# Optimization experiments

Hardware: AMD Instinct MI355X
Metric: run time of the kernel (lower is better)

Reference implementation:

```python
import jax, jax.numpy as jnp
import numpy as np

N_NODES = 50000
N_EDGES = 800000
IN_DIM = 128
HID = 256
OUT_DIM = 256
N_HEADS = 8
E_DIM = 64
KV_IN = 2 * IN_DIM + E_DIM  # 320


def _mlp_params(key, din, dhid, dout):
    k1, k2 = jax.random.split(key)
    s1 = 1.0 / np.sqrt(din)
    s2 = 1.0 / np.sqrt(dhid)
    return (jax.random.uniform(k1, (din, dhid), jnp.float32, -s1, s1),
            jnp.zeros((dhid,), jnp.float32),
            jax.random.uniform(k2, (dhid, dout), jnp.float32, -s2, s2),
            jnp.zeros((dout,), jnp.float32))


def setup_inputs() -> dict:
    key = jax.random.key(0)
    kh, ke, kidx, kk, kv, kq = jax.random.split(key, 6)
    h = jax.random.normal(kh, (N_NODES, IN_DIM), jnp.float32)
    e = jax.random.normal(ke, (N_EDGES, E_DIM), jnp.float32)
    edge_index = jax.random.randint(kidx, (2, N_EDGES), 0, N_NODES, jnp.int64)
    Wk1, bk1, Wk2, bk2 = _mlp_params(kk, KV_IN, HID, OUT_DIM)
    Wv1, bv1, Wv2, bv2 = _mlp_params(kv, KV_IN, HID, OUT_DIM)
    Wq1, bq1, Wq2, bq2 = _mlp_params(kq, IN_DIM, HID, OUT_DIM)
    return {"h": h, "e": e, "edge_index": edge_index,
            "Wk1": Wk1, "bk1": bk1, "Wk2": Wk2, "bk2": bk2,
            "Wv1": Wv1, "bv1": bv1, "Wv2": Wv2, "bv2": bv2,
            "Wq1": Wq1, "bq1": bq1, "Wq2": Wq2, "bq2": bq2}


def _mlp(x, W1, b1, W2, b2):
    # MLP(in, out, hidden, norm=False): Linear -> ReLU -> Linear
    return jax.nn.relu(x @ W1 + b1) @ W2 + b2


def reference(h, e, edge_index,
              Wk1, bk1, Wk2, bk2,
              Wv1, bv1, Wv2, bv2,
              Wq1, bq1, Wq2, bq2):
    N = h.shape[0]
    d_head = OUT_DIM // N_HEADS
    src, dst = edge_index[0], edge_index[1]
    # gather endpoints: hi = h[dst], hj = h[src]
    kv_input = jnp.concatenate([e, h[dst], h[src]], axis=-1)  # [E, KV_IN]
    k = _mlp(kv_input, Wk1, bk1, Wk2, bk2).reshape(-1, N_HEADS, d_head)
    v = _mlp(kv_input, Wv1, bv1, Wv2, bv2).reshape(-1, N_HEADS, d_head)
    q = _mlp(h, Wq1, bq1, Wq2, bq2).reshape(-1, N_HEADS, d_head)
    # per-edge logits, scaled dot product [E, H]
    logits = jnp.sum(q[dst] * k, axis=-1) * (1.0 / np.sqrt(d_head))
    # scatter softmax over destination groups
    mx = jax.ops.segment_max(logits, dst, num_segments=N)  # [N, H]
    ex = jnp.exp(logits - mx[dst])
    den = jax.ops.segment_sum(ex, dst, num_segments=N)  # [N, H]
    alpha = ex / den[dst]  # [E, H]
    # weighted scatter-sum aggregate
    m = alpha[..., None] * v  # [E, H, d_head]
    out = jax.ops.segment_sum(m, dst, num_segments=N)  # [N, H, d_head]
    return out.reshape(N, OUT_DIM)
```

## Files before the change

### kernel.cpp

```cpp
#include <hip/hip_runtime.h>

#define NND 50000
#define NE  800000
#define IND 128
#define HD  256
#define OD  256
#define NH  8
#define ED  64

typedef __attribute__((ext_vector_type(8))) short bf16x8;
typedef __attribute__((ext_vector_type(4))) float f32x4;

__device__ __forceinline__ float bf2f(unsigned short u) {
    union { unsigned int i; float f; } x; x.i = ((unsigned int)u) << 16; return x.f;
}
__device__ __forceinline__ unsigned short f2bf(float f) {
    union { float f; unsigned int i; } x; x.f = f;
    unsigned int u = x.i;
    u += 0x7FFFu + ((u >> 16) & 1u);
    return (unsigned short)(u >> 16);
}
__device__ __forceinline__ unsigned int pk2(float a, float b) {
    unsigned int r;
    asm("v_cvt_pk_bf16_f32 %0, %1, %2" : "=v"(r) : "v"(a), "v"(b));
    return r;
}

__global__ void k_hist(const int* __restrict__ eidx, int* __restrict__ cnt) {
    int e = blockIdx.x * 256 + threadIdx.x;
    if (e < NE) atomicAdd(&cnt[eidx[NE + e]], 1);
}

__global__ __launch_bounds__(1024) void k_scan(const int* __restrict__ cnt,
                                               int* __restrict__ head) {
    __shared__ int part[1024];
    const int t = threadIdx.x;
    const int CH = (NND + 1023) / 1024;
    int base = t * CH;
    int s = 0;
    for (int i = 0; i < CH; ++i) { int idx = base + i; if (idx < NND) s += cnt[idx]; }
    part[t] = s;
    __syncthreads();
    for (int off = 1; off < 1024; off <<= 1) {
        int v = (t >= off) ? part[t - off] : 0;
        __syncthreads();
        part[t] += v;
        __syncthreads();
    }
    int excl = (t == 0) ? 0 : part[t - 1];
    for (int i = 0; i < CH; ++i) {
        int idx = base + i; if (idx >= NND) break;
        head[idx] = excl;
        excl += cnt[idx];
    }
}

__global__ void k_scatter(const int* __restrict__ eidx, int* __restrict__ head,
                          int* __restrict__ perm, int* __restrict__ srcS,
                          int* __restrict__ dstS) {
    int e = blockIdx.x * 256 + threadIdx.x;
    if (e < NE) {
        int s = eidx[e];
        int d = eidx[NE + e];
        int pos = atomicAdd(&head[d], 1);
        perm[pos] = e;
        srcS[pos] = s;
        dstS[pos] = d;
    }
}

__device__ __forceinline__ void pack1(const float* __restrict__ W,
                                      unsigned short* __restrict__ P,
                                      int K, int N, int rowoff, int tid) {
    int j = tid & 7;
    int l = (tid >> 3) & 63;
    int rest = tid >> 9;
    int KS = K >> 5;
    int ks = rest % KS;
    int ct = rest / KS;
    int n = ct * 16 + (l & 15);
    int k = ks * 32 + (l >> 4) * 8 + j;
    P[tid] = f2bf(W[(size_t)(rowoff + k) * N + n]);
}

__global__ void k_packall(const float* __restrict__ Wq1, const float* __restrict__ Wq2,
                          const float* __restrict__ Wk1, const float* __restrict__ Wk2,
                          const float* __restrict__ Wv1, const float* __restrict__ Wv2,
                          unsigned short* __restrict__ Wq1p, unsigned short* __restrict__ Wq2p,
                          unsigned short* __restrict__ WeK,  unsigned short* __restrict__ W2K,
                          unsigned short* __restrict__ WdK,  unsigned short* __restrict__ WsK,
                          unsigned short* __restrict__ WeV,  unsigned short* __restrict__ W2V,
                          unsigned short* __restrict__ WdV,  unsigned short* __restrict__ WsV)
{
    int tid = blockIdx.x * 256 + threadIdx.x;
    int chunk = tid >> 14;
    if      (chunk < 2)   pack1(Wq1, Wq1p, 128, 256, 0,   tid);
    else if (chunk < 6)   pack1(Wq2, Wq2p, 256, 256, 0,   tid - (2 << 14));
    else if (chunk < 7)   pack1(Wk1, WeK,   64, 256, 0,   tid - (6 << 14));
    else if (chunk < 11)  pack1(Wk2, W2K,  256, 256, 0,   tid - (7 << 14));
    else if (chunk < 13)  pack1(Wk1, WdK,  128, 256, 64,  tid - (11 << 14));
    else if (chunk < 15)  pack1(Wk1, WsK,  128, 256, 192, tid - (13 << 14));
    else if (chunk < 16)  pack1(Wv1, WeV,   64, 256, 0,   tid - (15 << 14));
    else if (chunk < 20)  pack1(Wv2, W2V,  256, 256, 0,   tid - (16 << 14));
    else if (chunk < 22)  pack1(Wv1, WdV,  128, 256, 64,  tid - (20 << 14));
    else                  pack1(Wv1, WsV,  128, 256, 192, tid - (22 << 14));
}

__device__ __forceinline__ void zero_acc(f32x4 (&acc)[4][4]) {
    #pragma unroll
    for (int c = 0; c < 4; ++c)
        #pragma unroll
        for (int i = 0; i < 4; ++i)
            #pragma unroll
            for (int r = 0; r < 4; ++r) acc[c][i][r] = 0.f;
}

template<int KS, int STRIDE>
__device__ __forceinline__ void gemmT(const unsigned short* X,
                                      const unsigned short* __restrict__ Wp,
                                      int w, int l, f32x4 (&acc)[4][4]) {
    for (int ks = 0; ks < KS; ++ks) {
        bf16x8 wf[4], xf[4];
        #pragma unroll
        for (int c = 0; c < 4; ++c)
            wf[c] = *(const bf16x8*)(Wp + (((4 * w + c) * KS + ks) * 64 + l) * 8);
        #pragma unroll
        for (int i = 0; i < 4; ++i)
            xf[i] = *(const bf16x8*)(X + (i * 16 + (l & 15)) * STRIDE + ks * 32 + (l >> 4) * 8);
        #pragma unroll
        for (int c = 0; c < 4; ++c)
            #pragma unroll
            for (int i = 0; i < 4; ++i)
                acc[c][i] = __builtin_amdgcn_mfma_f32_16x16x32_bf16(wf[c], xf[i], acc[c][i], 0, 0, 0);
    }
}

__device__ __forceinline__ void lin_epi(const unsigned short* __restrict__ Wp,
                                        unsigned short* __restrict__ outp,
                                        const unsigned short* sXp,
                                        int w, int l, int g, int el, int m0) {
    f32x4 acc[4][4];
    zero_acc(acc);
    gemmT<4, 136>(sXp, Wp, w, l, acc);
    #pragma unroll
    for (int c = 0; c < 4; ++c) {
        int hid0 = 64 * w + 16 * c + 4 * g;
        #pragma unroll
        for (int i = 0; i < 4; ++i) {
            int node = m0 + 16 * i + el;
            if (node < NND) {
                uint2 pk;
                pk.x = pk2(acc[c][i][0], acc[c][i][1]);
                pk.y = pk2(acc[c][i][2], acc[c][i][3]);
                *(uint2*)(outp + (size_t)node * HD + hid0) = pk;
            }
        }
    }
}

__global__ __launch_bounds__(256) void k_node(
    const float* __restrict__ h,
    const unsigned short* __restrict__ Wq1p, const float* __restrict__ bq1,
    const unsigned short* __restrict__ Wq2p, const float* __restrict__ bq2,
    unsigned short* __restrict__ qb,
    const unsigned short* __restrict__ WdK, const unsigned short* __restrict__ WsK,
    const unsigned short* __restrict__ WdV, const unsigned short* __restrict__ WsV,
    unsigned short* __restrict__ udK, unsigned short* __restrict__ usK,
    unsigned short* __restrict__ udV, unsigned short* __restrict__ usV)
{
    __shared__ unsigned short sX[64][136];
    __shared__ unsigned short sH[64][264];
    const int t = threadIdx.x, w = t >> 6, l = t & 63;
    const int g = l >> 4, el = l & 15;
    const int m0 = blockIdx.x * 64;

    for (int c = t; c < 2048; c += 256) {
        int row = c >> 5, j = c & 31;
        int node = m0 + row; if (node >= NND) node = NND - 1;
        float4 v = *(const float4*)(h + (size_t)node * IND + j * 4);
        uint2 pk; pk.x = pk2(v.x, v.y); pk.y = pk2(v.z, v.w);
        *(uint2*)(&sX[row][j * 4]) = pk;
    }
    __syncthreads();

    f32x4 acc[4][4];
    zero_acc(acc);
    gemmT<4, 136>(&sX[0][0], Wq1p, w, l, acc);
    #pragma unroll
    for (int c = 0; c < 4; ++c) {
        int hid0 = 64 * w + 16 * c + 4 * g;
        float4 bv = *(const float4*)(bq1 + hid0);
        #pragma unroll
        for (int i = 0; i < 4; ++i) {
            uint2 pk;
            pk.x = pk2(fmaxf(acc[c][i][0] + bv.x, 0.f), fmaxf(acc[c][i][1] + bv.y, 0.f));
            pk.y = pk2(fmaxf(acc[c][i][2] + bv.z, 0.f), fmaxf(acc[c][i][3] + bv.w, 0.f));
            *(uint2*)(&sH[16 * i + el][hid0]) = pk;
        }
    }
    __syncthreads();

    zero_acc(acc);
    gemmT<8, 264>(&sH[0][0], Wq2p, w, l, acc);
    #pragma unroll
    for (int c = 0; c < 4; ++c) {
        int out0 = 64 * w + 16 * c + 4 * g;
        float4 bv = *(const float4*)(bq2 + out0);
        #pragma unroll
        for (int i = 0; i < 4; ++i) {
            int node = m0 + 16 * i + el;
            if (node < NND) {
                uint2 pk;
                pk.x = pk2(acc[c][i][0] + bv.x, acc[c][i][1] + bv.y);
                pk.y = pk2(acc[c][i][2] + bv.z, acc[c][i][3] + bv.w);
                *(uint2*)(qb + (size_t)node * OD + out0) = pk;
            }
        }
    }

    lin_epi(WdK, udK, &sX[0][0], w, l, g, el, m0);
    lin_epi(WsK, usK, &sX[0][0], w, l, g, el, m0);
    lin_epi(WdV, udV, &sX[0][0], w, l, g, el, m0);
    lin_epi(WsV, usV, &sX[0][0], w, l, g, el, m0);
}

struct SmF {
    unsigned short E[64][72];
    unsigned short H[64][264];
    int   Eid[64];
    int   Src[64];
    int   Dst[64];
    float Ex[64][9];
};

__device__ __forceinline__ void epi_pre(SmF& sm, f32x4 (&acc)[4][4],
                                        const float* __restrict__ b1,
                                        int w, int g, int el) {
    #pragma unroll
    for (int c = 0; c < 4; ++c) {
        int hid0 = 64 * w + 16 * c + 4 * g;
        float4 bv = *(const float4*)(b1 + hid0);
        #pragma unroll
        for (int i = 0; i < 4; ++i) {
            uint2 pk;
            pk.x = pk2(acc[c][i][0] + bv.x, acc[c][i][1] + bv.y);
            pk.y = pk2(acc[c][i][2] + bv.z, acc[c][i][3] + bv.w);
            *(uint2*)(&sm.H[16 * i + el][hid0]) = pk;
        }
    }
}

__device__ __forceinline__ void elemwise(SmF& sm,
                                         const unsigned short* __restrict__ ud,
                                         const unsigned short* __restrict__ us,
                                         int t) {
    int er = t >> 2;
    const unsigned short* udr = ud + (size_t)sm.Dst[er] * HD;
    const unsigned short* usr = us + (size_t)sm.Src[er] * HD;
    bf16x8 vd[8], vs[8];
    #pragma unroll
    for (int j = 0; j < 8; ++j) {
        int col = (j * 4 + (t & 3)) * 8;
        vd[j] = *(const bf16x8*)(udr + col);
        vs[j] = *(const bf16x8*)(usr + col);
    }
    #pragma unroll
    for (int j = 0; j < 8; ++j) {
        int col = (j * 4 + (t & 3)) * 8;
        bf16x8 hv = *(const bf16x8*)(&sm.H[er][col]);
        float x[8];
        #pragma unroll
        for (int u = 0; u < 8; ++u) {
            x[u] = bf2f((unsigned short)hv[u]) + bf2f((unsigned short)vd[j][u])
                 + bf2f((unsigned short)vs[j][u]);
            x[u] = fmaxf(x[u], 0.f);
        }
        uint4 o;
        o.x = pk2(x[0], x[1]); o.y = pk2(x[2], x[3]);
        o.z = pk2(x[4], x[5]); o.w = pk2(x[6], x[7]);
        *(uint4*)(&sm.H[er][col]) = o;
    }
}

__global__ __launch_bounds__(256, 3) void k_edgeF(
    const float* __restrict__ eattr,
    const int* __restrict__ perm,
    const int* __restrict__ srcS, const int* __restrict__ dstS,
    const unsigned short* __restrict__ WeK, const float* __restrict__ b1K,
    const unsigned short* __restrict__ W2K, const float* __restrict__ b2K,
    const unsigned short* __restrict__ WeV, const float* __restrict__ b1V,
    const unsigned short* __restrict__ W2V, const float* __restrict__ b2V,
    const unsigned short* __restrict__ udK, const unsigned short* __restrict__ usK,
    const unsigned short* __restrict__ udV, const unsigned short* __restrict__ usV,
    const unsigned short* __restrict__ qb,
    float* __restrict__ den, float* __restrict__ outp)
{
    __shared__ SmF sm;
    const int t = threadIdx.x, w = t >> 6, l = t & 63;
    const int g = l >> 4, el = l & 15;
    const int e0 = blockIdx.x * 64;

    if (t < 64) {
        sm.Eid[t] = perm[e0 + t];
        sm.Src[t] = srcS[e0 + t];
        sm.Dst[t] = dstS[e0 + t];
    }
    __syncthreads();
    for (int c = t; c < 1024; c += 256) {
        int row = c >> 4, j = c & 15;
        float4 v = *(const float4*)(eattr + (size_t)sm.Eid[row] * ED + j * 4);
        uint2 pk; pk.x = pk2(v.x, v.y); pk.y = pk2(v.z, v.w);
        *(uint2*)(&sm.E[row][j * 4]) = pk;
    }
    __syncthreads();

    f32x4 acc[4][4];

    zero_acc(acc);
    gemmT<2, 72>(&sm.E[0][0], WeK, w, l, acc);
    epi_pre(sm, acc, b1K, w, g, el);
    __syncthreads();
    elemwise(sm, udK, usK, t);
    __syncthreads();

    zero_acc(acc);
    gemmT<8, 264>(&sm.H[0][0], W2K, w, l, acc);
    __syncthreads();
    epi_pre(sm, acc, b2K, w, g, el);
    __syncthreads();

    {
        const float scale = 0.17677669529663687f;
        for (int p = t; p < 512; p += 256) {
            int er = p >> 3, hh = p & 7;
            int dn = sm.Dst[er];
            const unsigned short* qrow = qb + (size_t)dn * OD + hh * 32;
            float s = 0.f;
            #pragma unroll
            for (int jj = 0; jj < 32; jj += 8) {
                bf16x8 qv = *(const bf16x8*)(qrow + jj);
                bf16x8 kv = *(const bf16x8*)(&sm.H[er][hh * 32 + jj]);
                #pragma unroll
                for (int u = 0; u < 8; ++u)
                    s += bf2f((unsigned short)qv[u]) * bf2f((unsigned short)kv[u]);
            }
            float ex = __expf(s * scale);
            sm.Ex[er][hh] = ex;
            atomicAdd(&den[dn * NH + hh], ex);
        }
    }

    zero_acc(acc);
    gemmT<2, 72>(&sm.E[0][0], WeV, w, l, acc);
    __syncthreads();
    epi_pre(sm, acc, b1V, w, g, el);
    __syncthreads();
    elemwise(sm, udV, usV, t);
    __syncthreads();

    zero_acc(acc);
    gemmT<8, 264>(&sm.H[0][0], W2V, w, l, acc);
    __syncthreads();

    #pragma unroll
    for (int c = 0; c < 4; ++c) {
        int out0 = 64 * w + 16 * c + 4 * g;
        float4 bv = *(const float4*)(b2V + out0);
        int hh = out0 >> 5;
        #pragma unroll
        for (int i = 0; i < 4; ++i) {
            int edge = 16 * i + el;
            float ex = sm.Ex[edge][hh];
            uint2 pk;
            pk.x = pk2((acc[c][i][0] + bv.x) * ex, (acc[c][i][1] + bv.y) * ex);
            pk.y = pk2((acc[c][i][2] + bv.z) * ex, (acc[c][i][3] + bv.w) * ex);
            *(uint2*)(&sm.H[edge][out0]) = pk;
        }
    }
    __syncthreads();

    {
        float run = 0.f; int prev = sm.Dst[0];
        for (int er = 0; er < 64; ++er) {
            int dn = sm.Dst[er];
            if (dn != prev) {
                atomicAdd(outp + (size_t)prev * OD + t, run);
                run = 0.f; prev = dn;
            }
            run += bf2f(sm.H[er][t]);
        }
        atomicAdd(outp + (size_t)prev * OD + t, run);
    }
}

__global__ void k_norm(float* __restrict__ outp, const float* __restrict__ den) {
    int i = blockIdx.x * 256 + threadIdx.x;
    if (i >= NND * OD / 4) return;
    int node = i >> 6;
    int c4 = i & 63;
    int hh = (c4 >> 3);
    float d = den[node * NH + hh];
    float inv = d > 0.f ? 1.f / d : 0.f;
    float4 v = *(float4*)(outp + (size_t)i * 4);
    v.x *= inv; v.y *= inv; v.z *= inv; v.w *= inv;
    *(float4*)(outp + (size_t)i * 4) = v;
}

extern "C" void kernel_launch(void* const* d_in, const int* in_sizes, int n_in,
                              void* d_out, int out_size, void* d_ws, size_t ws_size,
                              hipStream_t stream)
{
    const float* h   = (const float*)d_in[0];
    const float* e   = (const float*)d_in[1];
    const int*   eid = (const int*)  d_in[2];
    const float* Wk1 = (const float*)d_in[3];
    const float* bk1 = (const float*)d_in[4];
    const float* Wk2 = (const float*)d_in[5];
    const float* bk2 = (const float*)d_in[6];
    const float* Wv1 = (const float*)d_in[7];
    const float* bv1 = (const float*)d_in[8];
    const float* Wv2 = (const float*)d_in[9];
    const float* bv2 = (const float*)d_in[10];
    const float* Wq1 = (const float*)d_in[11];
    const float* bq1 = (const float*)d_in[12];
    const float* Wq2 = (const float*)d_in[13];
    const float* bq2 = (const float*)d_in[14];

    char* ws = (char*)d_ws;
    size_t off = 0;
    auto take = [&](size_t bytes) { char* p = ws + off; off += bytes; return p; };
    unsigned short* qb   = (unsigned short*)take(25600000);
    unsigned short* udK  = (unsigned short*)take(25600000);
    unsigned short* usK  = (unsigned short*)take(25600000);
    unsigned short* udV  = (unsigned short*)take(25600000);
    unsigned short* usV  = (unsigned short*)take(25600000);
    float*          den  = (float*)         take(1600000);
    int*            cnt  = (int*)           take(200000);
    int*            head = (int*)           take(200000);
    int*            perm = (int*)           take(3200000);
    int*            srcS = (int*)           take(3200000);
    int*            dstS = (int*)           take(3200000);
    unsigned short* Wq1p = (unsigned short*)take(65536);
    unsigned short* Wq2p = (unsigned short*)take(131072);
    unsigned short* WeK  = (unsigned short*)take(32768);
    unsigned short* W2K  = (unsigned short*)take(131072);
    unsigned short* WdK  = (unsigned short*)take(65536);
    unsigned short* WsK  = (unsigned short*)take(65536);
    unsigned short* WeV  = (unsigned short*)take(32768);
    unsigned short* W2V  = (unsigned short*)take(131072);
    unsigned short* WdV  = (unsigned short*)take(65536);
    unsigned short* WsV  = (unsigned short*)take(65536);
    const size_t needed = off;
    if (ws_size < needed) return;

    hipMemsetAsync(d_out, 0, (size_t)NND * OD * sizeof(float), stream);
    hipMemsetAsync(den, 0, (size_t)NND * NH * sizeof(float), stream);
    hipMemsetAsync(cnt, 0, (size_t)NND * sizeof(int), stream);

    k_hist<<<(NE + 255) / 256, 256, 0, stream>>>(eid, cnt);
    k_scan<<<1, 1024, 0, stream>>>(cnt, head);
    k_scatter<<<(NE + 255) / 256, 256, 0, stream>>>(eid, head, perm, srcS, dstS);

    k_packall<<<(24 << 14) / 256, 256, 0, stream>>>(Wq1, Wq2, Wk1, Wk2, Wv1, Wv2,
                                                    Wq1p, Wq2p, WeK, W2K, WdK, WsK,
                                                    WeV, W2V, WdV, WsV);

    k_node<<<(NND + 63) / 64, 256, 0, stream>>>(h, Wq1p, bq1, Wq2p, bq2, qb,
                                                WdK, WsK, WdV, WsV,
                                                udK, usK, udV, usV);

    k_edgeF<<<NE / 64, 256, 0, stream>>>(e, perm, srcS, dstS,
                                         WeK, bk1, W2K, bk2,
                                         WeV, bv1, W2V, bv2,
                                         udK, usK, udV, usV,
                                         qb, den, (float*)d_out);

    k_norm<<<(NND * OD / 4 + 255) / 256, 256, 0, stream>>>((float*)d_out, den);
}
```

Measured before the change: 763.4 us.

## Run K and V MLP branches concurrently in 512-thread edge blocks

The edge kernel now launches 512 threads per block, and the two 4-wave halves compute the K and V MLP pipelines at the same time on separate shared-memory buffers, where before they ran one after the other. This aims to roughly halve the serial chain of GEMM and sync phases per block and to expose more parallelism per CU. In exchange shared memory per block grows by a second H buffer and register pressure comes under a 512/4 launch bound, which may lower occupancy. During the logit and aggregation phases the other half of the threads sit idle.

```diff
diff --git a/kernel.cpp b/kernel.cpp
--- a/kernel.cpp
+++ b/kernel.cpp
@@ -224,16 +224,16 @@
     lin_epi(WsV, usV, &sX[0][0], w, l, g, el, m0);
 }
 
-struct SmF {
+struct SmF2 {
     unsigned short E[64][72];
-    unsigned short H[64][264];
-    int   Eid[64];
+    unsigned short Hk[64][264];
+    unsigned short Hv[64][264];
     int   Src[64];
     int   Dst[64];
     float Ex[64][9];
 };
 
-__device__ __forceinline__ void epi_pre(SmF& sm, f32x4 (&acc)[4][4],
+__device__ __forceinline__ void epi_pre(unsigned short (*H)[264], f32x4 (&acc)[4][4],
                                         const float* __restrict__ b1,
                                         int w, int g, int el) {
     #pragma unroll
@@ -245,29 +245,29 @@
             uint2 pk;
             pk.x = pk2(acc[c][i][0] + bv.x, acc[c][i][1] + bv.y);
             pk.y = pk2(acc[c][i][2] + bv.z, acc[c][i][3] + bv.w);
-            *(uint2*)(&sm.H[16 * i + el][hid0]) = pk;
-        }
-    }
-}
-
-__device__ __forceinline__ void elemwise(SmF& sm,
+            *(uint2*)(&H[16 * i + el][hid0]) = pk;
+        }
+    }
+}
+
+__device__ __forceinline__ void elemwise(unsigned short (*H)[264],
                                          const unsigned short* __restrict__ ud,
                                          const unsigned short* __restrict__ us,
-                                         int t) {
-    int er = t >> 2;
-    const unsigned short* udr = ud + (size_t)sm.Dst[er] * HD;
-    const unsigned short* usr = us + (size_t)sm.Src[er] * HD;
+                                         const int* Src, const int* Dst, int tl) {
+    int er = tl >> 2;
+    const unsigned short* udr = ud + (size_t)Dst[er] * HD;
+    const unsigned short* usr = us + (size_t)Src[er] * HD;
     bf16x8 vd[8], vs[8];
     #pragma unroll
     for (int j = 0; j < 8; ++j) {
-        int col = (j * 4 + (t & 3)) * 8;
+        int col = (j * 4 + (tl & 3)) * 8;
         vd[j] = *(const bf16x8*)(udr + col);
         vs[j] = *(const bf16x8*)(usr + col);
     }
     #pragma unroll
     for (int j = 0; j < 8; ++j) {
-        int col = (j * 4 + (t & 3)) * 8;
-        bf16x8 hv = *(const bf16x8*)(&sm.H[er][col]);
+        int col = (j * 4 + (tl & 3)) * 8;
+        bf16x8 hv = *(const bf16x8*)(&H[er][col]);
         float x[8];
         #pragma unroll
         for (int u = 0; u < 8; ++u) {
@@ -278,11 +278,11 @@
         uint4 o;
         o.x = pk2(x[0], x[1]); o.y = pk2(x[2], x[3]);
         o.z = pk2(x[4], x[5]); o.w = pk2(x[6], x[7]);
-        *(uint4*)(&sm.H[er][col]) = o;
-    }
-}
-
-__global__ __launch_bounds__(256, 3) void k_edgeF(
+        *(uint4*)(&H[er][col]) = o;
+    }
+}
+
+__global__ __launch_bounds__(512, 4) void k_edgeF(
     const float* __restrict__ eattr,
     const int* __restrict__ perm,
     const int* __restrict__ srcS, const int* __restrict__ dstS,
@@ -295,41 +295,51 @@
     const unsigned short* __restrict__ qb,
     float* __restrict__ den, float* __restrict__ outp)
 {
-    __shared__ SmF sm;
+    __shared__ SmF2 sm;
     const int t = threadIdx.x, w = t >> 6, l = t & 63;
     const int g = l >> 4, el = l & 15;
+    const int role = w >> 2;
+    const int wl = w & 3;
+    const int tl = t & 255;
     const int e0 = blockIdx.x * 64;
 
+    const unsigned short* We = role ? WeV : WeK;
+    const float*          b1 = role ? b1V : b1K;
+    const unsigned short* W2 = role ? W2V : W2K;
+    const float*          b2 = role ? b2V : b2K;
+    const unsigned short* ud = role ? udV : udK;
+    const unsigned short* us = role ? usV : usK;
+    unsigned short (*H)[264] = role ? sm.Hv : sm.Hk;
+
     if (t < 64) {
-        sm.Eid[t] = perm[e0 + t];
         sm.Src[t] = srcS[e0 + t];
         sm.Dst[t] = dstS[e0 + t];
     }
-    __syncthreads();
-    for (int c = t; c < 1024; c += 256) {
+    for (int c = t; c < 1024; c += 512) {
         int row = c >> 4, j = c & 15;
-        float4 v = *(const float4*)(eattr + (size_t)sm.Eid[row] * ED + j * 4);
+        int eid = perm[e0 + row];
+        float4 v = *(const float4*)(eattr + (size_t)eid * ED + j * 4);
         uint2 pk; pk.x = pk2(v.x, v.y); pk.y = pk2(v.z, v.w);
         *(uint2*)(&sm.E[row][j * 4]) = pk;
     }
     __syncthreads();
 
     f32x4 acc[4][4];
-
     zero_acc(acc);
-    gemmT<2, 72>(&sm.E[0][0], WeK, w, l, acc);
-    epi_pre(sm, acc, b1K, w, g, el);
-    __syncthreads();
-    elemwise(sm, udK, usK, t);
-    __syncthreads();
-
+    gemmT<2, 72>(&sm.E[0][0], We, wl, l, acc);
+    epi_pre(H, acc, b1, wl, g, el);
+    __syncthreads();
+    elemwise(H, ud, us, sm.Src, sm.Dst, tl);
+    __syncthreads();
     zero_acc(acc);
-    gemmT<8, 264>(&sm.H[0][0], W2K, w, l, acc);
-    __syncthreads();
-    epi_pre(sm, acc, b2K, w, g, el);
-    __syncthreads();
-
-    {
+    gemmT<8, 264>(&H[0][0], W2, wl, l, acc);
+    __syncthreads();
+
+    if (role == 0)
+        epi_pre(sm.Hk, acc, b2, wl, g, el);
+    __syncthreads();
+
+    if (role == 0) {
         const float scale = 0.17677669529663687f;
         for (int p = t; p < 512; p += 256) {
             int er = p >> 3, hh = p & 7;
@@ -339,7 +349,7 @@
             #pragma unroll
             for (int jj = 0; jj < 32; jj += 8) {
                 bf16x8 qv = *(const bf16x8*)(qrow + jj);
-                bf16x8 kv = *(const bf16x8*)(&sm.H[er][hh * 32 + jj]);
+                bf16x8 kv = *(const bf16x8*)(&sm.Hk[er][hh * 32 + jj]);
                 #pragma unroll
                 for (int u = 0; u < 8; ++u)
                     s += bf2f((unsigned short)qv[u]) * bf2f((unsigned short)kv[u]);
@@ -349,37 +359,28 @@
             atomicAdd(&den[dn * NH + hh], ex);
         }
     }
-
-    zero_acc(acc);
-    gemmT<2, 72>(&sm.E[0][0], WeV, w, l, acc);
-    __syncthreads();
-    epi_pre(sm, acc, b1V, w, g, el);
-    __syncthreads();
-    elemwise(sm, udV, usV, t);
-    __syncthreads();
-
-    zero_acc(acc);
-    gemmT<8, 264>(&sm.H[0][0], W2V, w, l, acc);
-    __syncthreads();
-
-    #pragma unroll
-    for (int c = 0; c < 4; ++c) {
-        int out0 = 64 * w + 16 * c + 4 * g;
-        float4 bv = *(const float4*)(b2V + out0);
-        int hh = out0 >> 5;
-        #pragma unroll
-        for (int i = 0; i < 4; ++i) {
-            int edge = 16 * i + el;
-            float ex = sm.Ex[edge][hh];
-            uint2 pk;
-            pk.x = pk2((acc[c][i][0] + bv.x) * ex, (acc[c][i][1] + bv.y) * ex);
-            pk.y = pk2((acc[c][i][2] + bv.z) * ex, (acc[c][i][3] + bv.w) * ex);
-            *(uint2*)(&sm.H[edge][out0]) = pk;
-        }
-    }
-    __syncthreads();
-
-    {
+    __syncthreads();
+
+    if (role == 1) {
+        #pragma unroll
+        for (int c = 0; c < 4; ++c) {
+            int out0 = 64 * wl + 16 * c + 4 * g;
+            float4 bv = *(const float4*)(b2 + out0);
+            int hh = out0 >> 5;
+            #pragma unroll
+            for (int i = 0; i < 4; ++i) {
+                int edge = 16 * i + el;
+                float ex = sm.Ex[edge][hh];
+                uint2 pk;
+                pk.x = pk2((acc[c][i][0] + bv.x) * ex, (acc[c][i][1] + bv.y) * ex);
+                pk.y = pk2((acc[c][i][2] + bv.z) * ex, (acc[c][i][3] + bv.w) * ex);
+                *(uint2*)(&sm.Hv[edge][out0]) = pk;
+            }
+        }
+    }
+    __syncthreads();
+
+    if (t < 256) {
         float run = 0.f; int prev = sm.Dst[0];
         for (int er = 0; er < 64; ++er) {
             int dn = sm.Dst[er];
@@ -387,7 +388,7 @@
                 atomicAdd(outp + (size_t)prev * OD + t, run);
                 run = 0.f; prev = dn;
             }
-            run += bf2f(sm.H[er][t]);
+            run += bf2f(sm.Hv[er][t]);
         }
         atomicAdd(outp + (size_t)prev * OD + t, run);
     }
@@ -469,7 +470,7 @@
                                                 WdK, WsK, WdV, WsV,
                                                 udK, usK, udV, usV);
 
-    k_edgeF<<<NE / 64, 256, 0, stream>>>(e, perm, srcS, dstS,
+    k_edgeF<<<NE / 64, 512, 0, stream>>>(e, perm, srcS, dstS,
                                          WeK, bk1, W2K, bk2,
                                          WeV, bv1, W2V, bv2,
                                          udK, usK, udV, usV,
```

New measurement: 980.3 us. +28.4%, slower.
